# Performance work log

Hardware: AMD Instinct MI355X
Metric: run time of the kernel (lower is better)

Reference implementation:

```python
import jax, jax.numpy as jnp
import numpy as np

B, T, E, H = 8, 2048, 1024, 128

def setup_inputs() -> dict:
    key = jax.random.key(0)
    k1, k2, k3, k4 = jax.random.split(key, 4)
    s = 0.02
    return {
        "x":  jax.random.normal(k1, (B, T, E), dtype=jnp.float32),
        "Wq": jax.random.normal(k2, (E, H), dtype=jnp.float32) * s,
        "Wk": jax.random.normal(k3, (E, H), dtype=jnp.float32) * s,
        "Wv": jax.random.normal(k4, (E, H), dtype=jnp.float32) * s,
    }

def reference(x, Wq, Wk, Wv):
    # q,k,v: [B,T,H]
    q = jnp.einsum("bte,eh->bth", x, Wq)
    k = jnp.einsum("bte,eh->bth", x, Wk)
    v = jnp.einsum("bte,eh->bth", x, Wv)
    scale = jnp.asarray(q.shape[-1], q.dtype) ** -0.5
    wei = jnp.einsum("bqh,bkh->bqk", q, k) * scale  # [B,T,T]
    causal = jnp.tril(jnp.ones((wei.shape[1], wei.shape[2]), dtype=bool))
    wei = jnp.where(causal, wei, jnp.asarray(-jnp.inf, wei.dtype))
    wei = jax.nn.softmax(wei, axis=-1)
    # dropout_prob = 0.0 -> identity
    return jnp.einsum("bqk,bkh->bqh", wei, v)
```

## Files before the change

### kernel.cpp

```cpp
#include <hip/hip_runtime.h>

#define BB 8
#define TT 2048
#define EE 1024
#define HH 128

typedef __bf16 bf16;
typedef __attribute__((ext_vector_type(8))) __bf16 bf16x8;
typedef __attribute__((ext_vector_type(4))) __bf16 bf16x4;
typedef __attribute__((ext_vector_type(4))) float f32x4;
typedef __attribute__((ext_vector_type(16))) float f32x16;

__device__ __host__ inline int qb_off(int qb) {
  int h = qb >> 1;
  return qb + h * (h - 1) + ((qb & 1) ? h : 0);
}
#define NSLAB 72

__device__ inline void gload_lds16(const bf16* g, bf16* l) {
  __builtin_amdgcn_global_load_lds((const __attribute__((address_space(1))) unsigned int*)g,
                                   (__attribute__((address_space(3))) unsigned int*)l,
                                   16, 0, 0);
}

__global__ __launch_bounds__(256) void prep_kernel(const float* __restrict__ x,
                                                   bf16* __restrict__ xb,
                                                   const float* __restrict__ wq,
                                                   const float* __restrict__ wk,
                                                   const float* __restrict__ wv,
                                                   bf16* __restrict__ wt) {
  __shared__ float tile[64][65];
  const int bid = blockIdx.x;
  if (bid < 4096) {
    const size_t base = (size_t)bid * 4096 + threadIdx.x * 4;
#pragma unroll
    for (int j = 0; j < 4; ++j) {
      size_t idx = base + j * 1024;
      f32x4 xv = *(const f32x4*)(x + idx);
      bf16x4 xo;
#pragma unroll
      for (int i = 0; i < 4; ++i) xo[i] = (bf16)xv[i];
      *(bf16x4*)(xb + idx) = xo;
    }
  } else {
    const int id = bid - 4096;
    const int z = id >> 5;
    const int h0 = ((id >> 4) & 1) * 64;
    const int k0 = (id & 15) * 64;
    const float* w = (z == 0) ? wq : ((z == 1) ? wk : wv);
    const int c = threadIdx.x & 63;
    const int r0 = threadIdx.x >> 6;
#pragma unroll
    for (int i = 0; i < 16; ++i) {
      int tt = r0 + i * 4;
      tile[tt][c] = w[(size_t)(k0 + tt) * HH + h0 + c];
    }
    __syncthreads();
#pragma unroll
    for (int i = 0; i < 16; ++i) {
      int hh = r0 + i * 4;
      wt[((size_t)(z * HH + h0 + hh)) * EE + k0 + c] = (bf16)tile[c][hh];
    }
  }
}

__global__ __launch_bounds__(256) void gemm_kernel(const bf16* __restrict__ xb,
                                                   const bf16* __restrict__ wt,
                                                   bf16* __restrict__ q,
                                                   bf16* __restrict__ k,
                                                   bf16* __restrict__ v) {
  __shared__ bf16 As[2][128 * 32];
  __shared__ bf16 Bs[2][96 * 32];
  const int tid = threadIdx.x;
  const int lane = tid & 63;
  const int wave = tid >> 6;
  const int l16 = lane & 15;
  const int quad = lane >> 4;
  const int wm = wave & 1;
  const int wn = wave >> 1;
  const int bm = blockIdx.x;
  const int ntile = blockIdx.y;

  const int trow = tid >> 2;
  const int tsub = (tid & 3) * 8;
  const bf16* gA = xb + (size_t)(bm * 128 + trow) * EE + tsub;
  const bf16* gB = wt + (size_t)(ntile * 96 + trow) * EE + tsub;

  f32x4 acc[4][3];
#pragma unroll
  for (int rg = 0; rg < 4; ++rg)
#pragma unroll
    for (int nt = 0; nt < 3; ++nt) acc[rg][nt] = f32x4{0.f, 0.f, 0.f, 0.f};

  auto stage = [&](int bufi, int ks) {
    gload_lds16(gA + ks * 32, &As[bufi][wave * 512]);
    gload_lds16(gA + (size_t)64 * EE + ks * 32, &As[bufi][2048 + wave * 512]);
    gload_lds16(gB + ks * 32, &Bs[bufi][wave * 512]);
    if (tid < 128)
      gload_lds16(gB + (size_t)64 * EE + ks * 32, &Bs[bufi][2048 + wave * 512]);
  };

  stage(0, 0);
  __syncthreads();

  int buf = 0;
  for (int ks = 0; ks < EE / 32; ++ks) {
    if (ks < EE / 32 - 1) stage(buf ^ 1, ks + 1);

    bf16x8 af[4], bf_[3];
#pragma unroll
    for (int rg = 0; rg < 4; ++rg)
      af[rg] = *(const bf16x8*)&As[buf][(wm * 64 + rg * 16 + l16) * 32 + quad * 8];
#pragma unroll
    for (int nt = 0; nt < 3; ++nt)
      bf_[nt] = *(const bf16x8*)&Bs[buf][(wn * 48 + nt * 16 + l16) * 32 + quad * 8];
#pragma unroll
    for (int rg = 0; rg < 4; ++rg)
#pragma unroll
      for (int nt = 0; nt < 3; ++nt)
        acc[rg][nt] = __builtin_amdgcn_mfma_f32_16x16x32_bf16(af[rg], bf_[nt], acc[rg][nt], 0, 0, 0);

    __syncthreads();
    buf ^= 1;
  }

  bf16* outp[3] = {q, k, v};
#pragma unroll
  for (int rg = 0; rg < 4; ++rg)
#pragma unroll
    for (int nt = 0; nt < 3; ++nt) {
      int col = ntile * 96 + wn * 48 + nt * 16 + l16;
      int z = col >> 7;
      int n = col & 127;
#pragma unroll
      for (int r = 0; r < 4; ++r) {
        int row = bm * 128 + wm * 64 + rg * 16 + quad * 4 + r;
        outp[z][(size_t)row * HH + n] = (bf16)acc[rg][nt][r];
      }
    }
}

__global__ __launch_bounds__(256) void vtrans_kernel(const bf16* __restrict__ v,
                                                     bf16* __restrict__ vt) {
  __shared__ bf16 tile[64][65];
  const int b = blockIdx.x;
  const int t0 = blockIdx.y * 64;
  const int h0 = blockIdx.z * 64;
  const int c = threadIdx.x & 63;
  const int r0 = threadIdx.x >> 6;
#pragma unroll
  for (int i = 0; i < 16; ++i) {
    int tt = r0 + i * 4;
    tile[tt][c] = v[((size_t)(b * TT + t0 + tt)) * HH + h0 + c];
  }
  __syncthreads();
#pragma unroll
  for (int i = 0; i < 16; ++i) {
    int hh = r0 + i * 4;
    vt[((size_t)(b * HH + h0 + hh)) * TT + t0 + c] = tile[c][hh];
  }
}

__device__ __forceinline__ unsigned pk2(float a, float b) {
  union { __bf16 h[2]; unsigned u; } x;
  x.h[0] = (__bf16)a;
  x.h[1] = (__bf16)b;
  return x.u;
}

__device__ __forceinline__ void plswap(unsigned& a, unsigned& b) {
  asm volatile("v_permlane32_swap_b32 %0, %1" : "+v"(a), "+v"(b));
}

__global__ __launch_bounds__(256, 2) void flash_kernel(const bf16* __restrict__ q,
                                                       const bf16* __restrict__ k,
                                                       const bf16* __restrict__ vt,
                                                       bf16* __restrict__ opart,
                                                       float* __restrict__ lpart) {
  __shared__ bf16 Ks[2][64 * 128];
  __shared__ bf16 Vs[2][128 * 64];

  const int b = blockIdx.x & 7;
  int j = (NSLAB - 1) - (blockIdx.x >> 3);
  int qb = 0, ns = 1;
  while (j >= ns) { j -= ns; ++qb; ns = ((2 * qb + 1) >> 2) + 1; }
  const int s = j;
  const int kt0 = s * 4;
  const int kt1 = min(kt0 + 3, 2 * qb + 1);

  const int tid = threadIdx.x;
  const int lane = tid & 63;
  const int wave = tid >> 6;
  const int l32 = lane & 31;
  const int hi = lane >> 5;
  const int qrow = qb * 128 + wave * 32 + l32;
  const int kdiag = qb * 4 + wave;

  bf16x8 qf[8];
  {
    const bf16* qp = q + (size_t)(b * TT + qrow) * HH + hi * 8;
#pragma unroll
    for (int h16 = 0; h16 < 8; ++h16) qf[h16] = *(const bf16x8*)(qp + h16 * 16);
  }

  f32x16 O[4];
#pragma unroll
  for (int ht = 0; ht < 4; ++ht)
#pragma unroll
    for (int r = 0; r < 16; ++r) O[ht][r] = 0.f;
  float L = 0.f;

  const int krow_s = tid >> 4;
  const int kchk_s = (tid & 15) ^ (krow_s & 7);
  const int vrow_s = tid >> 3;
  const int vchk_s = (tid & 7) ^ (vrow_s & 7);
  const bf16* kg = k + (size_t)b * TT * HH;
  const bf16* vg = vt + (size_t)b * HH * TT;

  auto stageKV = [&](int bufi, int kt) {
#pragma unroll
    for (int i = 0; i < 4; ++i)
      gload_lds16(kg + (size_t)(kt * 64 + i * 16 + krow_s) * HH + kchk_s * 8,
                  &Ks[bufi][(i * 256 + wave * 64) * 8]);
#pragma unroll
    for (int i = 0; i < 4; ++i)
      gload_lds16(vg + (size_t)(i * 32 + vrow_s) * TT + kt * 64 + vchk_s * 8,
                  &Vs[bufi][(i * 256 + wave * 64) * 8]);
  };

  const int kxor = (l32 & 7) << 3;
  const float c_ = 0.12753257680406733f;

  stageKV(0, kt0);
  __syncthreads();

  int buf = 0;
  for (int kt = kt0; kt <= kt1; ++kt) {
    if (kt < kt1) stageKV(buf ^ 1, kt + 1);

#pragma unroll
    for (int khalf = 0; khalf < 2; ++khalf) {
      const int k32 = kt * 2 + khalf;
      if (k32 <= kdiag) {
        const bf16* kls = &Ks[buf][(khalf * 32 + l32) * 128];
        bf16x8 kf[8];
#pragma unroll
        for (int h16 = 0; h16 < 8; ++h16)
          kf[h16] = *(const bf16x8*)&kls[(h16 * 16 + hi * 8) ^ kxor];

        f32x16 S;
#pragma unroll
        for (int r = 0; r < 16; ++r) S[r] = 0.f;
        __builtin_amdgcn_s_setprio(1);
#pragma unroll
        for (int h16 = 0; h16 < 8; ++h16)
          S = __builtin_amdgcn_mfma_f32_32x32x16_bf16(kf[h16], qf[h16], S, 0, 0, 0);
        __builtin_amdgcn_s_setprio(0);

        float p[16];
        if (k32 == kdiag) {
          const int kkb = k32 * 32 + 4 * hi;
#pragma unroll
          for (int r = 0; r < 16; ++r) {
            int kk = kkb + (r & 3) + 8 * (r >> 2);
            float pv = (kk <= qrow) ? exp2f(S[r] * c_) : 0.f;
            p[r] = pv;
            L += pv;
          }
        } else {
#pragma unroll
          for (int r = 0; r < 16; ++r) {
            float pv = exp2f(S[r] * c_);
            p[r] = pv;
            L += pv;
          }
        }

#pragma unroll
        for (int s16 = 0; s16 < 2; ++s16) {
          unsigned w0 = pk2(p[s16 * 8 + 0], p[s16 * 8 + 1]);
          unsigned w1 = pk2(p[s16 * 8 + 2], p[s16 * 8 + 3]);
          unsigned w2 = pk2(p[s16 * 8 + 4], p[s16 * 8 + 5]);
          unsigned w3 = pk2(p[s16 * 8 + 6], p[s16 * 8 + 7]);
          plswap(w0, w2);
          plswap(w1, w3);
          union { unsigned u[4]; bf16x8 v; } af;
          af.u[0] = w0;
          af.u[1] = w1;
          af.u[2] = w2;
          af.u[3] = w3;
          bf16x8 vf[4];
#pragma unroll
          for (int ht = 0; ht < 4; ++ht)
            vf[ht] = *(const bf16x8*)&Vs[buf][(l32 + 32 * ht) * 64 +
                                             ((khalf * 32 + s16 * 16 + hi * 8) ^ kxor)];
          __builtin_amdgcn_s_setprio(1);
#pragma unroll
          for (int ht = 0; ht < 4; ++ht)
            O[ht] = __builtin_amdgcn_mfma_f32_32x32x16_bf16(af.v, vf[ht], O[ht], 0, 0, 0);
          __builtin_amdgcn_s_setprio(0);
        }
      }
    }
    __syncthreads();
    buf ^= 1;
  }

  L += __shfl_xor(L, 32, 64);

  const size_t slab = (size_t)(b * NSLAB + qb_off(qb) + s);
  bf16* op = opart + slab * (128 * 128) + (size_t)wave * 32 * 128;
#pragma unroll
  for (int ht = 0; ht < 4; ++ht)
#pragma unroll
    for (int r = 0; r < 16; ++r) {
      int qr = (r & 3) + 8 * (r >> 2) + 4 * hi;
      op[qr * 128 + ht * 32 + l32] = (bf16)O[ht][r];
    }
  if (hi == 0) lpart[slab * 128 + wave * 32 + l32] = L;
}

__global__ __launch_bounds__(128) void combine_kernel(const bf16* __restrict__ opart,
                                                      const float* __restrict__ lpart,
                                                      float* __restrict__ out) {
  const int b = blockIdx.x;
  const int qt16 = blockIdx.y;
  const int half = blockIdx.z;
  const int row = threadIdx.x >> 3;
  const int colo = (threadIdx.x & 7) * 8 + half * 64;
  const int qb = qt16 >> 3;
  const int srow = (qt16 & 7) * 16 + row;
  const int ns = ((2 * qb + 1) >> 2) + 1;
  const size_t slab0 = (size_t)(b * NSLAB + qb_off(qb));

  float acc[8];
#pragma unroll
  for (int j = 0; j < 8; ++j) acc[j] = 0.f;
  float L = 0.f;

  int s = 0;
  for (; s + 4 <= ns; s += 4) {
    float l0 = lpart[(slab0 + s + 0) * 128 + srow];
    float l1 = lpart[(slab0 + s + 1) * 128 + srow];
    float l2 = lpart[(slab0 + s + 2) * 128 + srow];
    float l3 = lpart[(slab0 + s + 3) * 128 + srow];
    bf16x8 v0 = *(const bf16x8*)(opart + (slab0 + s + 0) * (128 * 128) + srow * 128 + colo);
    bf16x8 v1 = *(const bf16x8*)(opart + (slab0 + s + 1) * (128 * 128) + srow * 128 + colo);
    bf16x8 v2 = *(const bf16x8*)(opart + (slab0 + s + 2) * (128 * 128) + srow * 128 + colo);
    bf16x8 v3 = *(const bf16x8*)(opart + (slab0 + s + 3) * (128 * 128) + srow * 128 + colo);
    L += (l0 + l1) + (l2 + l3);
#pragma unroll
    for (int j = 0; j < 8; ++j)
      acc[j] += ((float)v0[j] + (float)v1[j]) + ((float)v2[j] + (float)v3[j]);
  }
  for (; s < ns; ++s) {
    L += lpart[(slab0 + s) * 128 + srow];
    bf16x8 ov = *(const bf16x8*)(opart + (slab0 + s) * (128 * 128) + srow * 128 + colo);
#pragma unroll
    for (int j = 0; j < 8; ++j) acc[j] += (float)ov[j];
  }
  float invL = 1.f / L;
  float* o = out + ((size_t)(b * TT + qt16 * 16 + row)) * HH + colo;
  f32x4 o0, o1;
#pragma unroll
  for (int j = 0; j < 4; ++j) { o0[j] = acc[j] * invL; o1[j] = acc[j + 4] * invL; }
  *(f32x4*)o = o0;
  *(f32x4*)(o + 4) = o1;
}

extern "C" void kernel_launch(void* const* d_in, const int* in_sizes, int n_in,
                              void* d_out, int out_size, void* d_ws, size_t ws_size,
                              hipStream_t stream) {
  const float* x = (const float*)d_in[0];
  const float* wq = (const float*)d_in[1];
  const float* wk = (const float*)d_in[2];
  const float* wv = (const float*)d_in[3];
  float* out = (float*)d_out;

  char* ws = (char*)d_ws;
  const size_t NE = (size_t)BB * TT * HH;
  bf16* wt = (bf16*)ws;
  bf16* xb = (bf16*)(ws + (1 << 20));
  bf16* q = (bf16*)(ws + (33 << 20));
  bf16* k = q + NE;
  bf16* v = k + NE;
  bf16* vt = v + NE;
  bf16* opart = xb;
  float* lpart = (float*)(opart + (size_t)(BB * NSLAB) * 128 * 128);

  prep_kernel<<<dim3(4192), 256, 0, stream>>>(x, xb, wq, wk, wv, wt);
  gemm_kernel<<<dim3(128, 4), 256, 0, stream>>>(xb, wt, q, k, v);
  vtrans_kernel<<<dim3(8, 32, 2), 256, 0, stream>>>(v, vt);
  flash_kernel<<<dim3(576), 256, 0, stream>>>(q, k, vt, opart, lpart);
  combine_kernel<<<dim3(8, 128, 2), 128, 0, stream>>>(opart, lpart, out);
}
```

Baseline: 154.7 us.

## Fuse V transpose into GEMM epilogue and load V directly from global memory

The GEMM epilogue now writes V straight into transposed layout as packed 4-element stores, which removes the separate vtrans kernel launch and its extra global round trip. The flash kernel stops staging V through shared memory and instead loads V fragments from global memory into registers, issued around the QK MFMAs to hide latency. This halves LDS use, so launch bounds are raised to allow 3 blocks per CU. The cost is uncoalesced, strided (TT stride) global loads of V per wave with no reuse across waves, plus possible register pressure at the higher occupancy target.

```diff
diff --git a/kernel.cpp b/kernel.cpp
--- a/kernel.cpp
+++ b/kernel.cpp
@@ -68,7 +68,7 @@
                                                    const bf16* __restrict__ wt,
                                                    bf16* __restrict__ q,
                                                    bf16* __restrict__ k,
-                                                   bf16* __restrict__ v) {
+                                                   bf16* __restrict__ vt) {
   __shared__ bf16 As[2][128 * 32];
   __shared__ bf16 Bs[2][96 * 32];
   const int tid = threadIdx.x;
@@ -124,7 +124,6 @@
     buf ^= 1;
   }
 
-  bf16* outp[3] = {q, k, v};
 #pragma unroll
   for (int rg = 0; rg < 4; ++rg)
 #pragma unroll
@@ -132,33 +131,21 @@
       int col = ntile * 96 + wn * 48 + nt * 16 + l16;
       int z = col >> 7;
       int n = col & 127;
-#pragma unroll
-      for (int r = 0; r < 4; ++r) {
-        int row = bm * 128 + wm * 64 + rg * 16 + quad * 4 + r;
-        outp[z][(size_t)row * HH + n] = (bf16)acc[rg][nt][r];
+      int row0 = bm * 128 + wm * 64 + rg * 16 + quad * 4;
+      if (z == 2) {
+        int bb = row0 >> 11;
+        int t0 = row0 & (TT - 1);
+        bf16x4 pkv;
+#pragma unroll
+        for (int r = 0; r < 4; ++r) pkv[r] = (bf16)acc[rg][nt][r];
+        *(bf16x4*)&vt[((size_t)(bb * HH + n)) * TT + t0] = pkv;
+      } else {
+        bf16* op = (z == 0) ? q : k;
+#pragma unroll
+        for (int r = 0; r < 4; ++r)
+          op[(size_t)(row0 + r) * HH + n] = (bf16)acc[rg][nt][r];
       }
     }
-}
-
-__global__ __launch_bounds__(256) void vtrans_kernel(const bf16* __restrict__ v,
-                                                     bf16* __restrict__ vt) {
-  __shared__ bf16 tile[64][65];
-  const int b = blockIdx.x;
-  const int t0 = blockIdx.y * 64;
-  const int h0 = blockIdx.z * 64;
-  const int c = threadIdx.x & 63;
-  const int r0 = threadIdx.x >> 6;
-#pragma unroll
-  for (int i = 0; i < 16; ++i) {
-    int tt = r0 + i * 4;
-    tile[tt][c] = v[((size_t)(b * TT + t0 + tt)) * HH + h0 + c];
-  }
-  __syncthreads();
-#pragma unroll
-  for (int i = 0; i < 16; ++i) {
-    int hh = r0 + i * 4;
-    vt[((size_t)(b * HH + h0 + hh)) * TT + t0 + c] = tile[c][hh];
-  }
 }
 
 __device__ __forceinline__ unsigned pk2(float a, float b) {
@@ -172,13 +159,12 @@
   asm volatile("v_permlane32_swap_b32 %0, %1" : "+v"(a), "+v"(b));
 }
 
-__global__ __launch_bounds__(256, 2) void flash_kernel(const bf16* __restrict__ q,
+__global__ __launch_bounds__(256, 3) void flash_kernel(const bf16* __restrict__ q,
                                                        const bf16* __restrict__ k,
                                                        const bf16* __restrict__ vt,
                                                        bf16* __restrict__ opart,
                                                        float* __restrict__ lpart) {
   __shared__ bf16 Ks[2][64 * 128];
-  __shared__ bf16 Vs[2][128 * 64];
 
   const int b = blockIdx.x & 7;
   int j = (NSLAB - 1) - (blockIdx.x >> 3);
@@ -212,36 +198,36 @@
 
   const int krow_s = tid >> 4;
   const int kchk_s = (tid & 15) ^ (krow_s & 7);
-  const int vrow_s = tid >> 3;
-  const int vchk_s = (tid & 7) ^ (vrow_s & 7);
   const bf16* kg = k + (size_t)b * TT * HH;
-  const bf16* vg = vt + (size_t)b * HH * TT;
-
-  auto stageKV = [&](int bufi, int kt) {
+
+  auto stageK = [&](int bufi, int kt) {
 #pragma unroll
     for (int i = 0; i < 4; ++i)
       gload_lds16(kg + (size_t)(kt * 64 + i * 16 + krow_s) * HH + kchk_s * 8,
                   &Ks[bufi][(i * 256 + wave * 64) * 8]);
-#pragma unroll
-    for (int i = 0; i < 4; ++i)
-      gload_lds16(vg + (size_t)(i * 32 + vrow_s) * TT + kt * 64 + vchk_s * 8,
-                  &Vs[bufi][(i * 256 + wave * 64) * 8]);
   };
 
+  const bf16* vb_base = vt + ((size_t)b * HH + l32) * TT + hi * 8;
   const int kxor = (l32 & 7) << 3;
   const float c_ = 0.12753257680406733f;
 
-  stageKV(0, kt0);
+  stageK(0, kt0);
   __syncthreads();
 
   int buf = 0;
   for (int kt = kt0; kt <= kt1; ++kt) {
-    if (kt < kt1) stageKV(buf ^ 1, kt + 1);
+    if (kt < kt1) stageK(buf ^ 1, kt + 1);
 
 #pragma unroll
     for (int khalf = 0; khalf < 2; ++khalf) {
       const int k32 = kt * 2 + khalf;
       if (k32 <= kdiag) {
+        const bf16* vb = vb_base + (size_t)k32 * 32;
+        bf16x8 vf0[4];
+#pragma unroll
+        for (int ht = 0; ht < 4; ++ht)
+          vf0[ht] = *(const bf16x8*)(vb + (size_t)(ht * 32) * TT);
+
         const bf16* kls = &Ks[buf][(khalf * 32 + l32) * 128];
         bf16x8 kf[8];
 #pragma unroll
@@ -256,6 +242,11 @@
         for (int h16 = 0; h16 < 8; ++h16)
           S = __builtin_amdgcn_mfma_f32_32x32x16_bf16(kf[h16], qf[h16], S, 0, 0, 0);
         __builtin_amdgcn_s_setprio(0);
+
+        bf16x8 vf1[4];
+#pragma unroll
+        for (int ht = 0; ht < 4; ++ht)
+          vf1[ht] = *(const bf16x8*)(vb + (size_t)(ht * 32) * TT + 16);
 
         float p[16];
         if (k32 == kdiag) {
@@ -289,15 +280,11 @@
           af.u[1] = w1;
           af.u[2] = w2;
           af.u[3] = w3;
-          bf16x8 vf[4];
+          __builtin_amdgcn_s_setprio(1);
 #pragma unroll
           for (int ht = 0; ht < 4; ++ht)
-            vf[ht] = *(const bf16x8*)&Vs[buf][(l32 + 32 * ht) * 64 +
-                                             ((khalf * 32 + s16 * 16 + hi * 8) ^ kxor)];
-          __builtin_amdgcn_s_setprio(1);
-#pragma unroll
-          for (int ht = 0; ht < 4; ++ht)
-            O[ht] = __builtin_amdgcn_mfma_f32_32x32x16_bf16(af.v, vf[ht], O[ht], 0, 0, 0);
+            O[ht] = __builtin_amdgcn_mfma_f32_32x32x16_bf16(
+                af.v, (s16 == 0) ? vf0[ht] : vf1[ht], O[ht], 0, 0, 0);
           __builtin_amdgcn_s_setprio(0);
         }
       }
@@ -383,14 +370,12 @@
   bf16* xb = (bf16*)(ws + (1 << 20));
   bf16* q = (bf16*)(ws + (33 << 20));
   bf16* k = q + NE;
-  bf16* v = k + NE;
-  bf16* vt = v + NE;
+  bf16* vt = k + NE;
   bf16* opart = xb;
   float* lpart = (float*)(opart + (size_t)(BB * NSLAB) * 128 * 128);
 
   prep_kernel<<<dim3(4192), 256, 0, stream>>>(x, xb, wq, wk, wv, wt);
-  gemm_kernel<<<dim3(128, 4), 256, 0, stream>>>(xb, wt, q, k, v);
-  vtrans_kernel<<<dim3(8, 32, 2), 256, 0, stream>>>(v, vt);
+  gemm_kernel<<<dim3(128, 4), 256, 0, stream>>>(xb, wt, q, k, vt);
   flash_kernel<<<dim3(576), 256, 0, stream>>>(q, k, vt, opart, lpart);
   combine_kernel<<<dim3(8, 128, 2), 128, 0, stream>>>(opart, lpart, out);
 }
```

Measured after the change: 188.4 us. 21.8% more time.
